# Performance work log

Hardware: AMD Instinct MI355X
Metric: run time of the kernel (lower is better)

Reference implementation:

```python
import jax, jax.numpy as jnp
import numpy as np

B, T, K = 256, 64, 512


def setup_inputs() -> dict:
    key = jax.random.key(0)
    k1, k2, k3, k4, k5 = jax.random.split(key, 5)
    return {
        "x": jax.random.uniform(k1, (B, T), dtype=jnp.float32),          # soft binary evidence
        "prior_w": jax.random.normal(k2, (K,), dtype=jnp.float32),
        "emission_w": jax.random.normal(k3, (K, 2), dtype=jnp.float32),
        "coeff": jax.random.normal(k4, (K, K), dtype=jnp.float32),
        "bias": jax.random.normal(k5, (K, K), dtype=jnp.float32),
    }


def reference(x, prior_w, emission_w, coeff, bias):
    # emission: per-row softmax of [K,2] raw weights (TF loops rows; equivalent to axis=1 softmax)
    emission = jax.nn.softmax(emission_w, axis=1)  # [K, 2]

    def evidence(h, xt):
        # h: [B,K] (or broadcastable [1,K]); xt: [B]
        aug = jnp.stack([1.0 - xt, xt], axis=1)          # [B, 2]
        e = aug @ emission.T                             # [B, K]
        p = h * e                                        # [B, K]
        return p / jnp.sum(p, axis=1, keepdims=True)     # row-normalize (get_normalized_pr)

    prior = jax.nn.softmax(prior_w)                      # [K]
    post0 = evidence(prior[None, :], x[:, 0])            # [B, K]

    def step(post, xt):
        # transition_raw[i,j,k] = post[i,j]*coeff[j,k] + bias[j,k]
        raw = post[:, :, None] * coeff[None, :, :] + bias[None, :, :]   # [B, K, K]
        trans = jax.nn.softmax(raw, axis=2)              # get_normalized_pr_with_batch
        pbe = jnp.einsum('ij,ijk->ik', post, trans)      # [B, K]
        return evidence(pbe, xt), None

    post, _ = jax.lax.scan(step, post0, x[:, 1:].T)      # scan over time steps 1..T-1
    return post
```

## Files before the change

kernel.cpp:

```cpp
#include <hip/hip_runtime.h>

#define KDIM 512
#define TDIM 64
#define NWAVE 16
#define BLOCK 1024
#define LOG2E 1.4426950408889634f

#define WS_B2     0
#define WS_XCHG   (KDIM * KDIM)
#define WS_FLAGS  (WS_XCHG + 128 * 2 * 2 * 1024)
#define WS_FLOATS (WS_FLAGS + 256)

__device__ __forceinline__ float fast_exp2(float v) { return __builtin_amdgcn_exp2f(v); }
__device__ __forceinline__ float fast_rcp(float v)  { return __builtin_amdgcn_rcpf(v); }

__global__ __launch_bounds__(256) void prefold_kernel(
    const float* __restrict__ bias, float* __restrict__ b2)
{
    const int i = blockIdx.x * 256 + threadIdx.x;
    const float4 b = ((const float4*)bias)[i];
    ((float4*)b2)[i] = make_float4(b.x * LOG2E, b.y * LOG2E, b.z * LOG2E, b.w * LOG2E);
}

__device__ __forceinline__ float wave_reduce_sum(float v) {
    #pragma unroll
    for (int off = 1; off < 64; off <<= 1)
        v += __shfl_xor(v, off, 64);
    return v;
}

__global__ __launch_bounds__(BLOCK)
__attribute__((amdgpu_waves_per_eu(4, 4)))
void hmm_pair_kernel(
    const float* __restrict__ x,
    const float* __restrict__ prior_w,
    const float* __restrict__ emission_w,
    const float* __restrict__ coeff,
    float* __restrict__ ws,
    float* __restrict__ out)
{
    __shared__ float post[2][KDIM];
    __shared__ float em0s[KDIM];
    __shared__ float emds[KDIM];
    __shared__ float part[NWAVE][2][KDIM];
    __shared__ float rtmp[NWAVE];
    __shared__ float rn2[2];
    __shared__ float xs[2][TDIM];

    const int gid  = blockIdx.x;
    const int h    = gid & 1;
    const int pair = gid >> 1;
    const int b0   = gid & ~1;
    const int tid  = threadIdx.x;
    const int lane = tid & 63;
    const int wv   = tid >> 6;
    const int k0   = 4 * lane;
    const int u    = tid >> 9;
    const int k    = tid & 511;

    const float* bb = ws + WS_B2;
    int* flags   = (int*)(ws + WS_FLAGS);
    int* my_flag = flags + (pair * 2 + h);
    int* pr_flag = flags + (pair * 2 + (1 - h));
    float* my_slot = ws + WS_XCHG + (size_t)(pair * 2 + h) * 2048;
    float* pr_slot = ws + WS_XCHG + (size_t)(pair * 2 + (1 - h)) * 2048;

    if (tid < 2 * TDIM) xs[tid >> 6][tid & 63] = x[(b0 + (tid >> 6)) * TDIM + (tid & 63)];
    if (tid < KDIM) {
        const float w0 = emission_w[2 * tid + 0];
        const float w1 = emission_w[2 * tid + 1];
        const float e0 = 1.0f / (1.0f + fast_exp2((w1 - w0) * LOG2E));
        em0s[tid] = e0;
        emds[tid] = 1.0f - 2.0f * e0;
    }
    __syncthreads();

    {
        const float x0 = xs[u][0];
        const float pr = fast_exp2(prior_w[k] * LOG2E);
        float v = pr * fmaf(x0, emds[k], em0s[k]);
        float s = wave_reduce_sum(v);
        if (lane == 0) rtmp[wv] = s;
        __syncthreads();
        if (wv < 2) {
            float t2 = (lane < 8) ? rtmp[wv * 8 + lane] : 0.0f;
            t2 += __shfl_xor(t2, 1, 64);
            t2 += __shfl_xor(t2, 2, 64);
            t2 += __shfl_xor(t2, 4, 64);
            if (lane == 0) rn2[wv] = fast_rcp(t2);
        }
        __syncthreads();
        post[u][k] = v * rn2[u];
        __syncthreads();
    }

    for (int t = 1; t < TDIM; ++t) {
        float acc[2][8];
        #pragma unroll
        for (int uu = 0; uu < 2; ++uu)
            #pragma unroll
            for (int q = 0; q < 8; ++q) acc[uu][q] = 0.0f;

        const float* cW = coeff + (size_t)(h * 256 + wv) * KDIM + k0;
        const float* bW = bb    + (size_t)(h * 256 + wv) * KDIM + k0;

        #pragma unroll 1
        for (int i = 0; i < 8; ++i) {
            const int jA = h * 256 + wv + 32 * i;
            const float* cA = cW + (size_t)(32 * i) * KDIM;
            const float* bA = bW + (size_t)(32 * i) * KDIM;
            const float* cB = cA + 16 * KDIM;
            const float* bB = bA + 16 * KDIM;
            const float4 cA0 = *(const float4*)cA;
            const float4 cA1 = *(const float4*)(cA + 256);
            const float4 bA0 = *(const float4*)bA;
            const float4 bA1 = *(const float4*)(bA + 256);
            const float4 cB0 = *(const float4*)cB;
            const float4 cB1 = *(const float4*)(cB + 256);
            const float4 bB0 = *(const float4*)bB;
            const float4 bB1 = *(const float4*)(bB + 256);

            #pragma unroll
            for (int uu = 0; uu < 2; ++uu) {
                const float pA  = post[uu][jA];
                const float pB  = post[uu][jA + 16];
                const float pAL = pA * LOG2E;
                const float pBL = pB * LOG2E;

                const float eA0 = fast_exp2(fmaf(pAL, cA0.x, bA0.x));
                const float eA1 = fast_exp2(fmaf(pAL, cA0.y, bA0.y));
                const float eA2 = fast_exp2(fmaf(pAL, cA0.z, bA0.z));
                const float eA3 = fast_exp2(fmaf(pAL, cA0.w, bA0.w));
                const float eA4 = fast_exp2(fmaf(pAL, cA1.x, bA1.x));
                const float eA5 = fast_exp2(fmaf(pAL, cA1.y, bA1.y));
                const float eA6 = fast_exp2(fmaf(pAL, cA1.z, bA1.z));
                const float eA7 = fast_exp2(fmaf(pAL, cA1.w, bA1.w));
                const float eB0 = fast_exp2(fmaf(pBL, cB0.x, bB0.x));
                const float eB1 = fast_exp2(fmaf(pBL, cB0.y, bB0.y));
                const float eB2 = fast_exp2(fmaf(pBL, cB0.z, bB0.z));
                const float eB3 = fast_exp2(fmaf(pBL, cB0.w, bB0.w));
                const float eB4 = fast_exp2(fmaf(pBL, cB1.x, bB1.x));
                const float eB5 = fast_exp2(fmaf(pBL, cB1.y, bB1.y));
                const float eB6 = fast_exp2(fmaf(pBL, cB1.z, bB1.z));
                const float eB7 = fast_exp2(fmaf(pBL, cB1.w, bB1.w));

                float sA = ((eA0 + eA1) + (eA2 + eA3)) + ((eA4 + eA5) + (eA6 + eA7));
                float sB = ((eB0 + eB1) + (eB2 + eB3)) + ((eB4 + eB5) + (eB6 + eB7));
                #pragma unroll
                for (int off = 1; off < 64; off <<= 1) {
                    sA += __shfl_xor(sA, off, 64);
                    sB += __shfl_xor(sB, off, 64);
                }
                const float scA = pA * fast_rcp(sA);
                const float scB = pB * fast_rcp(sB);

                acc[uu][0] = fmaf(scA, eA0, acc[uu][0]); acc[uu][0] = fmaf(scB, eB0, acc[uu][0]);
                acc[uu][1] = fmaf(scA, eA1, acc[uu][1]); acc[uu][1] = fmaf(scB, eB1, acc[uu][1]);
                acc[uu][2] = fmaf(scA, eA2, acc[uu][2]); acc[uu][2] = fmaf(scB, eB2, acc[uu][2]);
                acc[uu][3] = fmaf(scA, eA3, acc[uu][3]); acc[uu][3] = fmaf(scB, eB3, acc[uu][3]);
                acc[uu][4] = fmaf(scA, eA4, acc[uu][4]); acc[uu][4] = fmaf(scB, eB4, acc[uu][4]);
                acc[uu][5] = fmaf(scA, eA5, acc[uu][5]); acc[uu][5] = fmaf(scB, eB5, acc[uu][5]);
                acc[uu][6] = fmaf(scA, eA6, acc[uu][6]); acc[uu][6] = fmaf(scB, eB6, acc[uu][6]);
                acc[uu][7] = fmaf(scA, eA7, acc[uu][7]); acc[uu][7] = fmaf(scB, eB7, acc[uu][7]);
            }
        }

        *(float4*)(&part[wv][0][k0])       = make_float4(acc[0][0], acc[0][1], acc[0][2], acc[0][3]);
        *(float4*)(&part[wv][0][256 + k0]) = make_float4(acc[0][4], acc[0][5], acc[0][6], acc[0][7]);
        *(float4*)(&part[wv][1][k0])       = make_float4(acc[1][0], acc[1][1], acc[1][2], acc[1][3]);
        *(float4*)(&part[wv][1][256 + k0]) = make_float4(acc[1][4], acc[1][5], acc[1][6], acc[1][7]);
        __syncthreads();

        float pbe = 0.0f;
        #pragma unroll
        for (int w2 = 0; w2 < NWAVE; ++w2) pbe += part[w2][u][k];

        float* slot = my_slot + (t & 1) * 1024;
        __hip_atomic_store(&slot[tid], pbe, __ATOMIC_RELAXED, __HIP_MEMORY_SCOPE_AGENT);
        __syncthreads();
        if (tid == 0) {
            __hip_atomic_store(my_flag, t, __ATOMIC_RELEASE, __HIP_MEMORY_SCOPE_AGENT);
            int f = __hip_atomic_load(pr_flag, __ATOMIC_ACQUIRE, __HIP_MEMORY_SCOPE_AGENT);
            while (f < t) {
                __builtin_amdgcn_s_sleep(8);
                f = __hip_atomic_load(pr_flag, __ATOMIC_ACQUIRE, __HIP_MEMORY_SCOPE_AGENT);
            }
        }
        __syncthreads();
        const float* pslot = pr_slot + (t & 1) * 1024;
        const float other = __hip_atomic_load(&pslot[tid], __ATOMIC_RELAXED, __HIP_MEMORY_SCOPE_AGENT);

        float v = (pbe + other) * fmaf(xs[u][t], emds[k], em0s[k]);
        float s = wave_reduce_sum(v);
        if (lane == 0) rtmp[wv] = s;
        __syncthreads();
        if (wv < 2) {
            float t2 = (lane < 8) ? rtmp[wv * 8 + lane] : 0.0f;
            t2 += __shfl_xor(t2, 1, 64);
            t2 += __shfl_xor(t2, 2, 64);
            t2 += __shfl_xor(t2, 4, 64);
            if (lane == 0) rn2[wv] = fast_rcp(t2);
        }
        __syncthreads();
        post[u][k] = v * rn2[u];
        __syncthreads();
    }

    if (tid < KDIM) out[(size_t)gid * KDIM + tid] = post[h][tid];
}

__global__ __launch_bounds__(BLOCK)
__attribute__((amdgpu_waves_per_eu(4, 4)))
void hmm_forward_kernel(
    const float* __restrict__ x, const float* __restrict__ prior_w,
    const float* __restrict__ emission_w, const float* __restrict__ coeff,
    const float* __restrict__ bias, float* __restrict__ out)
{
    __shared__ float post[KDIM];
    __shared__ float em0s[KDIM];
    __shared__ float emds[KDIM];
    __shared__ float part[NWAVE][KDIM];
    __shared__ float rtmp[NWAVE];
    __shared__ float xs[TDIM];

    const int b = blockIdx.x, tid = threadIdx.x, lane = tid & 63, wv = tid >> 6;
    const int k0 = 4 * lane;

    if (tid < TDIM) xs[tid] = x[b * TDIM + tid];
    if (tid < KDIM) {
        const float w0 = emission_w[2 * tid + 0];
        const float w1 = emission_w[2 * tid + 1];
        const float e0 = 1.0f / (1.0f + fast_exp2((w1 - w0) * LOG2E));
        em0s[tid] = e0;
        emds[tid] = 1.0f - 2.0f * e0;
    }
    __syncthreads();
    {
        const float x0 = xs[0];
        float v = 0.0f;
        if (tid < KDIM)
            v = fast_exp2(prior_w[tid] * LOG2E) * fmaf(x0, emds[tid], em0s[tid]);
        float s = wave_reduce_sum(v);
        if (lane == 0) rtmp[wv] = s;
        __syncthreads();
        if (wv == 0) {
            float t2 = (lane < NWAVE) ? rtmp[lane] : 0.0f;
            #pragma unroll
            for (int off = 1; off < NWAVE; off <<= 1) t2 += __shfl_xor(t2, off, 64);
            if (lane == 0) rtmp[0] = t2;
        }
        __syncthreads();
        const float rn = fast_rcp(rtmp[0]);
        if (tid < KDIM) post[tid] = v * rn;
        __syncthreads();
    }
    for (int t = 1; t < TDIM; ++t) {
        float acc[8];
        #pragma unroll
        for (int i = 0; i < 8; ++i) acc[i] = 0.0f;
        const float* cA = coeff + (size_t)wv * KDIM + k0;
        const float* bA = bias  + (size_t)wv * KDIM + k0;
        const float* cB = cA + 16 * KDIM;
        const float* bB = bA + 16 * KDIM;
        #pragma unroll 1
        for (int i = 0; i < 16; ++i) {
            const float4 cA0 = *(const float4*)cA;
            const float4 cA1 = *(const float4*)(cA + 256);
            const float4 cB0 = *(const float4*)cB;
            const float4 cB1 = *(const float4*)(cB + 256);
            const float4 bA0 = *(const float4*)bA;
            const float4 bA1 = *(const float4*)(bA + 256);
            const float4 bB0 = *(const float4*)bB;
            const float4 bB1 = *(const float4*)(bB + 256);
            cA += 32 * KDIM; cB += 32 * KDIM; bA += 32 * KDIM; bB += 32 * KDIM;
            const float pA = post[wv + 32 * i];
            const float pB = post[wv + 16 + 32 * i];
            const float eA0 = fast_exp2(fmaf(pA, cA0.x, bA0.x) * LOG2E);
            const float eA1 = fast_exp2(fmaf(pA, cA0.y, bA0.y) * LOG2E);
            const float eA2 = fast_exp2(fmaf(pA, cA0.z, bA0.z) * LOG2E);
            const float eA3 = fast_exp2(fmaf(pA, cA0.w, bA0.w) * LOG2E);
            const float eA4 = fast_exp2(fmaf(pA, cA1.x, bA1.x) * LOG2E);
            const float eA5 = fast_exp2(fmaf(pA, cA1.y, bA1.y) * LOG2E);
            const float eA6 = fast_exp2(fmaf(pA, cA1.z, bA1.z) * LOG2E);
            const float eA7 = fast_exp2(fmaf(pA, cA1.w, bA1.w) * LOG2E);
            const float eB0 = fast_exp2(fmaf(pB, cB0.x, bB0.x) * LOG2E);
            const float eB1 = fast_exp2(fmaf(pB, cB0.y, bB0.y) * LOG2E);
            const float eB2 = fast_exp2(fmaf(pB, cB0.z, bB0.z) * LOG2E);
            const float eB3 = fast_exp2(fmaf(pB, cB0.w, bB0.w) * LOG2E);
            const float eB4 = fast_exp2(fmaf(pB, cB1.x, bB1.x) * LOG2E);
            const float eB5 = fast_exp2(fmaf(pB, cB1.y, bB1.y) * LOG2E);
            const float eB6 = fast_exp2(fmaf(pB, cB1.z, bB1.z) * LOG2E);
            const float eB7 = fast_exp2(fmaf(pB, cB1.w, bB1.w) * LOG2E);
            float sA = ((eA0 + eA1) + (eA2 + eA3)) + ((eA4 + eA5) + (eA6 + eA7));
            float sB = ((eB0 + eB1) + (eB2 + eB3)) + ((eB4 + eB5) + (eB6 + eB7));
            #pragma unroll
            for (int off = 1; off < 64; off <<= 1) {
                sA += __shfl_xor(sA, off, 64);
                sB += __shfl_xor(sB, off, 64);
            }
            const float scA = pA * fast_rcp(sA);
            const float scB = pB * fast_rcp(sB);
            acc[0] = fmaf(scA, eA0, acc[0]); acc[0] = fmaf(scB, eB0, acc[0]);
            acc[1] = fmaf(scA, eA1, acc[1]); acc[1] = fmaf(scB, eB1, acc[1]);
            acc[2] = fmaf(scA, eA2, acc[2]); acc[2] = fmaf(scB, eB2, acc[2]);
            acc[3] = fmaf(scA, eA3, acc[3]); acc[3] = fmaf(scB, eB3, acc[3]);
            acc[4] = fmaf(scA, eA4, acc[4]); acc[4] = fmaf(scB, eB4, acc[4]);
            acc[5] = fmaf(scA, eA5, acc[5]); acc[5] = fmaf(scB, eB5, acc[5]);
            acc[6] = fmaf(scA, eA6, acc[6]); acc[6] = fmaf(scB, eB6, acc[6]);
            acc[7] = fmaf(scA, eA7, acc[7]); acc[7] = fmaf(scB, eB7, acc[7]);
        }
        *(float4*)(&part[wv][k0])       = make_float4(acc[0], acc[1], acc[2], acc[3]);
        *(float4*)(&part[wv][256 + k0]) = make_float4(acc[4], acc[5], acc[6], acc[7]);
        __syncthreads();
        float v = 0.0f;
        if (tid < KDIM) {
            float pbe = 0.0f;
            #pragma unroll
            for (int w2 = 0; w2 < NWAVE; ++w2) pbe += part[w2][tid];
            v = pbe * fmaf(xs[t], emds[tid], em0s[tid]);
        }
        float s = wave_reduce_sum(v);
        if (lane == 0) rtmp[wv] = s;
        __syncthreads();
        if (wv == 0) {
            float t2 = (lane < NWAVE) ? rtmp[lane] : 0.0f;
            #pragma unroll
            for (int off = 1; off < NWAVE; off <<= 1) t2 += __shfl_xor(t2, off, 64);
            if (lane == 0) rtmp[0] = t2;
        }
        __syncthreads();
        const float rn = fast_rcp(rtmp[0]);
        if (tid < KDIM) post[tid] = v * rn;
        __syncthreads();
    }
    if (tid < KDIM) out[b * KDIM + tid] = post[tid];
}

extern "C" void kernel_launch(void* const* d_in, const int* in_sizes, int n_in,
                              void* d_out, int out_size, void* d_ws, size_t ws_size,
                              hipStream_t stream) {
    const float* x          = (const float*)d_in[0];
    const float* prior_w    = (const float*)d_in[1];
    const float* emission_w = (const float*)d_in[2];
    const float* coeff      = (const float*)d_in[3];
    const float* bias       = (const float*)d_in[4];
    float* out              = (float*)d_out;

    if (ws_size >= (size_t)WS_FLOATS * sizeof(float)) {
        float* ws = (float*)d_ws;
        hipLaunchKernelGGL(prefold_kernel, dim3(KDIM * KDIM / 4 / 256), dim3(256),
                           0, stream, bias, ws + WS_B2);
        hipLaunchKernelGGL(hmm_pair_kernel, dim3(256), dim3(BLOCK), 0, stream,
                           x, prior_w, emission_w, coeff, ws, out);
    } else {
        hipLaunchKernelGGL(hmm_forward_kernel, dim3(256), dim3(BLOCK), 0, stream,
                           x, prior_w, emission_w, coeff, bias, out);
    }
}
```

Before: 1.201 ms.

## Vectorize pair kernel with packed float2 math and batch shuffle reductions

Rewrites the inner transition loop of the pair kernel to use two-wide vector types, so the FMAs and accumulations can map to packed FP32 instructions. The four wave-level shuffle reductions are interleaved into one loop for more instruction-level parallelism. It also drops a barrier and the rn2 stage by having every thread sum the eight per-wave partials itself, and cuts the spin-wait sleep on the partner flag from 8 to 1. Block-to-pair mapping changes so the two halves of a pair are 128 blocks apart rather than adjacent, which alters co-residency and L2 locality. Register pressure may rise from holding all exponentials before the reductions.

```diff
diff --git a/kernel.cpp b/kernel.cpp
--- a/kernel.cpp
+++ b/kernel.cpp
@@ -5,6 +5,8 @@
 #define NWAVE 16
 #define BLOCK 1024
 #define LOG2E 1.4426950408889634f
+
+typedef float v2f __attribute__((ext_vector_type(2)));
 
 #define WS_B2     0
 #define WS_XCHG   (KDIM * KDIM)
@@ -44,13 +46,12 @@
     __shared__ float emds[KDIM];
     __shared__ float part[NWAVE][2][KDIM];
     __shared__ float rtmp[NWAVE];
-    __shared__ float rn2[2];
     __shared__ float xs[2][TDIM];
 
     const int gid  = blockIdx.x;
-    const int h    = gid & 1;
-    const int pair = gid >> 1;
-    const int b0   = gid & ~1;
+    const int pair = gid & 127;
+    const int h    = gid >> 7;
+    const int b0   = 2 * pair;
     const int tid  = threadIdx.x;
     const int lane = tid & 63;
     const int wv   = tid >> 6;
@@ -77,98 +78,97 @@
 
     {
         const float x0 = xs[u][0];
-        const float pr = fast_exp2(prior_w[k] * LOG2E);
-        float v = pr * fmaf(x0, emds[k], em0s[k]);
+        float v = fast_exp2(prior_w[k] * LOG2E) * fmaf(x0, emds[k], em0s[k]);
         float s = wave_reduce_sum(v);
         if (lane == 0) rtmp[wv] = s;
         __syncthreads();
-        if (wv < 2) {
-            float t2 = (lane < 8) ? rtmp[wv * 8 + lane] : 0.0f;
-            t2 += __shfl_xor(t2, 1, 64);
-            t2 += __shfl_xor(t2, 2, 64);
-            t2 += __shfl_xor(t2, 4, 64);
-            if (lane == 0) rn2[wv] = fast_rcp(t2);
-        }
-        __syncthreads();
-        post[u][k] = v * rn2[u];
+        const float* rb = &rtmp[u * 8];
+        const float tot = ((rb[0] + rb[1]) + (rb[2] + rb[3]))
+                        + ((rb[4] + rb[5]) + (rb[6] + rb[7]));
+        post[u][k] = v * fast_rcp(tot);
         __syncthreads();
     }
 
     for (int t = 1; t < TDIM; ++t) {
-        float acc[2][8];
+        v2f acc[2][4];
         #pragma unroll
         for (int uu = 0; uu < 2; ++uu)
             #pragma unroll
-            for (int q = 0; q < 8; ++q) acc[uu][q] = 0.0f;
-
-        const float* cW = coeff + (size_t)(h * 256 + wv) * KDIM + k0;
-        const float* bW = bb    + (size_t)(h * 256 + wv) * KDIM + k0;
+            for (int q = 0; q < 4; ++q) acc[uu][q] = (v2f){0.0f, 0.0f};
+
+        const float* pc = coeff + (size_t)(h * 256 + wv) * KDIM + k0;
+        const float* pb = bb    + (size_t)(h * 256 + wv) * KDIM + k0;
 
         #pragma unroll 1
         for (int i = 0; i < 8; ++i) {
             const int jA = h * 256 + wv + 32 * i;
-            const float* cA = cW + (size_t)(32 * i) * KDIM;
-            const float* bA = bW + (size_t)(32 * i) * KDIM;
-            const float* cB = cA + 16 * KDIM;
-            const float* bB = bA + 16 * KDIM;
-            const float4 cA0 = *(const float4*)cA;
-            const float4 cA1 = *(const float4*)(cA + 256);
-            const float4 bA0 = *(const float4*)bA;
-            const float4 bA1 = *(const float4*)(bA + 256);
-            const float4 cB0 = *(const float4*)cB;
-            const float4 cB1 = *(const float4*)(cB + 256);
-            const float4 bB0 = *(const float4*)bB;
-            const float4 bB1 = *(const float4*)(bB + 256);
-
+            const float4 cA0 = *(const float4*)pc;
+            const float4 cA1 = *(const float4*)(pc + 256);
+            const float4 cB0 = *(const float4*)(pc + 16 * KDIM);
+            const float4 cB1 = *(const float4*)(pc + 16 * KDIM + 256);
+            const float4 bA0 = *(const float4*)pb;
+            const float4 bA1 = *(const float4*)(pb + 256);
+            const float4 bB0 = *(const float4*)(pb + 16 * KDIM);
+            const float4 bB1 = *(const float4*)(pb + 16 * KDIM + 256);
+            pc += 32 * KDIM; pb += 32 * KDIM;
+
+            const v2f cav[4] = {{cA0.x, cA0.y}, {cA0.z, cA0.w}, {cA1.x, cA1.y}, {cA1.z, cA1.w}};
+            const v2f cbv[4] = {{cB0.x, cB0.y}, {cB0.z, cB0.w}, {cB1.x, cB1.y}, {cB1.z, cB1.w}};
+            const v2f bav[4] = {{bA0.x, bA0.y}, {bA0.z, bA0.w}, {bA1.x, bA1.y}, {bA1.z, bA1.w}};
+            const v2f bbv[4] = {{bB0.x, bB0.y}, {bB0.z, bB0.w}, {bB1.x, bB1.y}, {bB1.z, bB1.w}};
+
+            float p[2][2];
+            p[0][0] = post[0][jA]; p[0][1] = post[0][jA + 16];
+            p[1][0] = post[1][jA]; p[1][1] = post[1][jA + 16];
+
+            v2f ev[2][2][4];
+            float s[4];
             #pragma unroll
             for (int uu = 0; uu < 2; ++uu) {
-                const float pA  = post[uu][jA];
-                const float pB  = post[uu][jA + 16];
-                const float pAL = pA * LOG2E;
-                const float pBL = pB * LOG2E;
-
-                const float eA0 = fast_exp2(fmaf(pAL, cA0.x, bA0.x));
-                const float eA1 = fast_exp2(fmaf(pAL, cA0.y, bA0.y));
-                const float eA2 = fast_exp2(fmaf(pAL, cA0.z, bA0.z));
-                const float eA3 = fast_exp2(fmaf(pAL, cA0.w, bA0.w));
-                const float eA4 = fast_exp2(fmaf(pAL, cA1.x, bA1.x));
-                const float eA5 = fast_exp2(fmaf(pAL, cA1.y, bA1.y));
-                const float eA6 = fast_exp2(fmaf(pAL, cA1.z, bA1.z));
-                const float eA7 = fast_exp2(fmaf(pAL, cA1.w, bA1.w));
-                const float eB0 = fast_exp2(fmaf(pBL, cB0.x, bB0.x));
-                const float eB1 = fast_exp2(fmaf(pBL, cB0.y, bB0.y));
-                const float eB2 = fast_exp2(fmaf(pBL, cB0.z, bB0.z));
-                const float eB3 = fast_exp2(fmaf(pBL, cB0.w, bB0.w));
-                const float eB4 = fast_exp2(fmaf(pBL, cB1.x, bB1.x));
-                const float eB5 = fast_exp2(fmaf(pBL, cB1.y, bB1.y));
-                const float eB6 = fast_exp2(fmaf(pBL, cB1.z, bB1.z));
-                const float eB7 = fast_exp2(fmaf(pBL, cB1.w, bB1.w));
-
-                float sA = ((eA0 + eA1) + (eA2 + eA3)) + ((eA4 + eA5) + (eA6 + eA7));
-                float sB = ((eB0 + eB1) + (eB2 + eB3)) + ((eB4 + eB5) + (eB6 + eB7));
+                const float pAL = p[uu][0] * LOG2E;
+                const float pBL = p[uu][1] * LOG2E;
+                const v2f pAv = {pAL, pAL};
+                const v2f pBv = {pBL, pBL};
                 #pragma unroll
-                for (int off = 1; off < 64; off <<= 1) {
-                    sA += __shfl_xor(sA, off, 64);
-                    sB += __shfl_xor(sB, off, 64);
+                for (int q = 0; q < 4; ++q) {
+                    const v2f aA = __builtin_elementwise_fma(pAv, cav[q], bav[q]);
+                    const v2f aB = __builtin_elementwise_fma(pBv, cbv[q], bbv[q]);
+                    v2f eA, eB;
+                    eA.x = fast_exp2(aA.x); eA.y = fast_exp2(aA.y);
+                    eB.x = fast_exp2(aB.x); eB.y = fast_exp2(aB.y);
+                    ev[uu][0][q] = eA;
+                    ev[uu][1][q] = eB;
                 }
-                const float scA = pA * fast_rcp(sA);
-                const float scB = pB * fast_rcp(sB);
-
-                acc[uu][0] = fmaf(scA, eA0, acc[uu][0]); acc[uu][0] = fmaf(scB, eB0, acc[uu][0]);
-                acc[uu][1] = fmaf(scA, eA1, acc[uu][1]); acc[uu][1] = fmaf(scB, eB1, acc[uu][1]);
-                acc[uu][2] = fmaf(scA, eA2, acc[uu][2]); acc[uu][2] = fmaf(scB, eB2, acc[uu][2]);
-                acc[uu][3] = fmaf(scA, eA3, acc[uu][3]); acc[uu][3] = fmaf(scB, eB3, acc[uu][3]);
-                acc[uu][4] = fmaf(scA, eA4, acc[uu][4]); acc[uu][4] = fmaf(scB, eB4, acc[uu][4]);
-                acc[uu][5] = fmaf(scA, eA5, acc[uu][5]); acc[uu][5] = fmaf(scB, eB5, acc[uu][5]);
-                acc[uu][6] = fmaf(scA, eA6, acc[uu][6]); acc[uu][6] = fmaf(scB, eB6, acc[uu][6]);
-                acc[uu][7] = fmaf(scA, eA7, acc[uu][7]); acc[uu][7] = fmaf(scB, eB7, acc[uu][7]);
-            }
-        }
-
-        *(float4*)(&part[wv][0][k0])       = make_float4(acc[0][0], acc[0][1], acc[0][2], acc[0][3]);
-        *(float4*)(&part[wv][0][256 + k0]) = make_float4(acc[0][4], acc[0][5], acc[0][6], acc[0][7]);
-        *(float4*)(&part[wv][1][k0])       = make_float4(acc[1][0], acc[1][1], acc[1][2], acc[1][3]);
-        *(float4*)(&part[wv][1][256 + k0]) = make_float4(acc[1][4], acc[1][5], acc[1][6], acc[1][7]);
+                const v2f tA = (ev[uu][0][0] + ev[uu][0][1]) + (ev[uu][0][2] + ev[uu][0][3]);
+                const v2f tB = (ev[uu][1][0] + ev[uu][1][1]) + (ev[uu][1][2] + ev[uu][1][3]);
+                s[uu * 2 + 0] = tA.x + tA.y;
+                s[uu * 2 + 1] = tB.x + tB.y;
+            }
+            #pragma unroll
+            for (int off = 1; off < 64; off <<= 1) {
+                s[0] += __shfl_xor(s[0], off, 64);
+                s[1] += __shfl_xor(s[1], off, 64);
+                s[2] += __shfl_xor(s[2], off, 64);
+                s[3] += __shfl_xor(s[3], off, 64);
+            }
+            #pragma unroll
+            for (int uu = 0; uu < 2; ++uu) {
+                const float scA = p[uu][0] * fast_rcp(s[uu * 2 + 0]);
+                const float scB = p[uu][1] * fast_rcp(s[uu * 2 + 1]);
+                const v2f scAv = {scA, scA};
+                const v2f scBv = {scB, scB};
+                #pragma unroll
+                for (int q = 0; q < 4; ++q) {
+                    acc[uu][q] = __builtin_elementwise_fma(scAv, ev[uu][0][q], acc[uu][q]);
+                    acc[uu][q] = __builtin_elementwise_fma(scBv, ev[uu][1][q], acc[uu][q]);
+                }
+            }
+        }
+
+        *(float4*)(&part[wv][0][k0])       = make_float4(acc[0][0].x, acc[0][0].y, acc[0][1].x, acc[0][1].y);
+        *(float4*)(&part[wv][0][256 + k0]) = make_float4(acc[0][2].x, acc[0][2].y, acc[0][3].x, acc[0][3].y);
+        *(float4*)(&part[wv][1][k0])       = make_float4(acc[1][0].x, acc[1][0].y, acc[1][1].x, acc[1][1].y);
+        *(float4*)(&part[wv][1][256 + k0]) = make_float4(acc[1][2].x, acc[1][2].y, acc[1][3].x, acc[1][3].y);
         __syncthreads();
 
         float pbe = 0.0f;
@@ -182,7 +182,7 @@
             __hip_atomic_store(my_flag, t, __ATOMIC_RELEASE, __HIP_MEMORY_SCOPE_AGENT);
             int f = __hip_atomic_load(pr_flag, __ATOMIC_ACQUIRE, __HIP_MEMORY_SCOPE_AGENT);
             while (f < t) {
-                __builtin_amdgcn_s_sleep(8);
+                __builtin_amdgcn_s_sleep(1);
                 f = __hip_atomic_load(pr_flag, __ATOMIC_ACQUIRE, __HIP_MEMORY_SCOPE_AGENT);
             }
         }
@@ -194,19 +194,14 @@
         float s = wave_reduce_sum(v);
         if (lane == 0) rtmp[wv] = s;
         __syncthreads();
-        if (wv < 2) {
-            float t2 = (lane < 8) ? rtmp[wv * 8 + lane] : 0.0f;
-            t2 += __shfl_xor(t2, 1, 64);
-            t2 += __shfl_xor(t2, 2, 64);
-            t2 += __shfl_xor(t2, 4, 64);
-            if (lane == 0) rn2[wv] = fast_rcp(t2);
-        }
-        __syncthreads();
-        post[u][k] = v * rn2[u];
-        __syncthreads();
-    }
-
-    if (tid < KDIM) out[(size_t)gid * KDIM + tid] = post[h][tid];
+        const float* rb = &rtmp[u * 8];
+        const float tot = ((rb[0] + rb[1]) + (rb[2] + rb[3]))
+                        + ((rb[4] + rb[5]) + (rb[6] + rb[7]));
+        post[u][k] = v * fast_rcp(tot);
+        __syncthreads();
+    }
+
+    if (tid < KDIM) out[(size_t)(b0 + h) * KDIM + tid] = post[h][tid];
 }
 
 __global__ __launch_bounds__(BLOCK)
@@ -260,19 +255,17 @@
         for (int i = 0; i < 8; ++i) acc[i] = 0.0f;
         const float* cA = coeff + (size_t)wv * KDIM + k0;
         const float* bA = bias  + (size_t)wv * KDIM + k0;
-        const float* cB = cA + 16 * KDIM;
-        const float* bB = bA + 16 * KDIM;
         #pragma unroll 1
         for (int i = 0; i < 16; ++i) {
             const float4 cA0 = *(const float4*)cA;
             const float4 cA1 = *(const float4*)(cA + 256);
-            const float4 cB0 = *(const float4*)cB;
-            const float4 cB1 = *(const float4*)(cB + 256);
+            const float4 cB0 = *(const float4*)(cA + 16 * KDIM);
+            const float4 cB1 = *(const float4*)(cA + 16 * KDIM + 256);
             const float4 bA0 = *(const float4*)bA;
             const float4 bA1 = *(const float4*)(bA + 256);
-            const float4 bB0 = *(const float4*)bB;
-            const float4 bB1 = *(const float4*)(bB + 256);
-            cA += 32 * KDIM; cB += 32 * KDIM; bA += 32 * KDIM; bB += 32 * KDIM;
+            const float4 bB0 = *(const float4*)(bA + 16 * KDIM);
+            const float4 bB1 = *(const float4*)(bA + 16 * KDIM + 256);
+            cA += 32 * KDIM; bA += 32 * KDIM;
             const float pA = post[wv + 32 * i];
             const float pB = post[wv + 16 + 32 * i];
             const float eA0 = fast_exp2(fmaf(pA, cA0.x, bA0.x) * LOG2E);
```

Measured after the change: 1.134 ms. -5.5%, faster.
